# Performance work log

Hardware: AMD Instinct MI355X
Metric: run time of the kernel (lower is better)

Reference implementation:

```python
import jax, jax.numpy as jnp
import numpy as np

N_NODES = 100000
N_EDGES = 1600000
IN_DIM = 128
OUT_DIM = 64


def setup_inputs() -> dict:
    key = jax.random.key(0)
    k = jax.random.split(key, 6)
    h = jax.random.normal(k[0], (N_NODES, IN_DIM), dtype=jnp.float32)
    W_fc = jax.random.normal(k[1], (IN_DIM, OUT_DIM), dtype=jnp.float32) / np.float32(np.sqrt(IN_DIM))
    W_attn = jax.random.normal(k[2], (2 * OUT_DIM, 1), dtype=jnp.float32) / np.float32(np.sqrt(2 * OUT_DIM))
    W_edge = jax.random.normal(k[3], (2 * OUT_DIM, OUT_DIM), dtype=jnp.float32) / np.float32(np.sqrt(2 * OUT_DIM))
    src = jax.random.randint(k[4], (N_EDGES,), 0, N_NODES, dtype=jnp.int32)
    dst = jax.random.randint(k[5], (N_EDGES,), 0, N_NODES, dtype=jnp.int32)
    return {"h": h, "W_fc": W_fc, "W_attn": W_attn, "W_edge": W_edge, "src": src, "dst": dst}


def reference(h, W_fc, W_attn, W_edge, src, dst):
    # node projection: z = fc(h)
    z = h @ W_fc                                   # [N, out_dim]
    # gather per-edge src/dst features and concat (edge_type == 0 branch)
    z2 = jnp.concatenate([z[src], z[dst]], axis=1)  # [E, 2*out_dim]
    a = (z2 @ W_attn)[:, 0]                         # [E] attention logits
    e = z2 @ W_edge                                 # [E, out_dim] edge messages
    # segment softmax over incoming edges of each destination node
    a_max = jax.ops.segment_max(a, dst, num_segments=N_NODES)   # [N]
    w = jnp.exp(a - a_max[dst])                                  # [E]
    denom = jax.ops.segment_sum(w, dst, num_segments=N_NODES)    # [N]
    alpha = w / denom[dst]                                       # [E]
    # weighted scatter-add of neighbor features + sum of edge messages
    h1 = jax.ops.segment_sum(alpha[:, None] * z[src], dst, num_segments=N_NODES)
    h2 = jax.ops.segment_sum(e, dst, num_segments=N_NODES)
    return h1 + h2
```

## Files before the change

kernel.cpp:

```cpp
#include <hip/hip_runtime.h>

#define IN_DIM 128
#define OUT_DIM 64

#define NB 256
#define BSHIFT 9
#define NPB 512
#define EPT 16

typedef __attribute__((ext_vector_type(8))) short short8;
typedef __attribute__((ext_vector_type(4))) float f32x4;

__device__ __forceinline__ unsigned pack_bf16x2(float a, float b) {
    unsigned ua = __float_as_uint(a), ub = __float_as_uint(b);
    ua = (ua + 0x7fffu + ((ua >> 16) & 1u)) >> 16;
    ub = (ub + 0x7fffu + ((ub >> 16) & 1u)) >> 16;
    return ua | (ub << 16);
}

__global__ void precompute_weights(const float* __restrict__ W_fc,
                                   const float* __restrict__ W_edge,
                                   float* __restrict__ W1, float* __restrict__ W2) {
    int k = blockIdx.x;
    int j = threadIdx.x;
    __shared__ float row[64];
    row[j] = W_fc[k * 64 + j];
    __syncthreads();
    float s1 = 0.f, s2 = 0.f;
    #pragma unroll 8
    for (int m = 0; m < 64; ++m) {
        float w = row[m];
        s1 = fmaf(w, W_edge[m * 64 + j], s1);
        s2 = fmaf(w, W_edge[(64 + m) * 64 + j], s2);
    }
    W1[k * 64 + j] = s1;
    W2[k * 64 + j] = s2;
}

__global__ void pack_bfrags(const float* __restrict__ W_fc, const float* __restrict__ W1,
                            const float* __restrict__ W2, unsigned* __restrict__ bfrag) {
    int slot = blockIdx.x * 256 + threadIdx.x;
    if (slot >= 12 * 4 * 64) return;
    int lane = slot & 63;
    int ks = (slot >> 6) & 3;
    int t = slot >> 8;
    int grp = t >> 2;
    int col = (t & 3) * 16 + (lane & 15);
    int kbase = ks * 32 + (lane >> 4) * 8;
    const float* W = (grp == 0) ? W_fc : ((grp == 1) ? W1 : W2);
    unsigned o0 = pack_bf16x2(W[(kbase + 0) * 64 + col], W[(kbase + 1) * 64 + col]);
    unsigned o1 = pack_bf16x2(W[(kbase + 2) * 64 + col], W[(kbase + 3) * 64 + col]);
    unsigned o2 = pack_bf16x2(W[(kbase + 4) * 64 + col], W[(kbase + 5) * 64 + col]);
    unsigned o3 = pack_bf16x2(W[(kbase + 6) * 64 + col], W[(kbase + 7) * 64 + col]);
    ((uint4*)bfrag)[slot] = make_uint4(o0, o1, o2, o3);
}

__global__ __launch_bounds__(256) void node_gemm(
    const float* __restrict__ h, const unsigned* __restrict__ bfrag,
    const float* __restrict__ W_attn,
    unsigned* __restrict__ zes, float* __restrict__ ed,
    float* __restrict__ ws_, int N)
{
    __shared__ uint4 lds4[1024];
    char* lds = (char*)lds4;
    const int tid = threadIdx.x;
    const int lane = tid & 63;
    const int w = tid >> 6;
    const int n0 = blockIdx.x * 64;

    #pragma unroll
    for (int r = 0; r < 8; ++r) {
        int idx = r * 256 + tid;
        int row = idx >> 5;
        int c4 = idx & 31;
        float4 v = make_float4(0.f, 0.f, 0.f, 0.f);
        int n = n0 + row;
        if (n < N) v = *(const float4*)(h + (size_t)n * IN_DIM + c4 * 4);
        int byte = (row << 8) + (c4 << 3);
        byte ^= ((row & 7) << 4);
        *(uint2*)(lds + byte) = make_uint2(pack_bf16x2(v.x, v.y), pack_bf16x2(v.z, v.w));
    }
    __syncthreads();

    const int g = lane >> 4;
    const int c = lane & 15;

    union U { uint4 u; short8 s; };
    U a[4];
    {
        const int arow = (w << 4) + c;
        #pragma unroll
        for (int ks = 0; ks < 4; ++ks) {
            int byte = (arow << 8) + (ks << 6) + (g << 4);
            byte ^= ((arow & 7) << 4);
            a[ks].u = *(const uint4*)(lds + byte);
        }
    }

    f32x4 acc[12];
    #pragma unroll
    for (int t = 0; t < 12; ++t) acc[t] = (f32x4){0.f, 0.f, 0.f, 0.f};

    const uint4* bf4 = (const uint4*)bfrag;
    #pragma unroll
    for (int t = 0; t < 12; ++t) {
        #pragma unroll
        for (int ks = 0; ks < 4; ++ks) {
            U b; b.u = bf4[(t * 4 + ks) * 64 + lane];
            acc[t] = __builtin_amdgcn_mfma_f32_16x16x32_bf16(a[ks].s, b.s, acc[t], 0, 0, 0);
        }
    }

    const float wa0 = W_attn[c], wa1 = W_attn[16 + c], wa2 = W_attn[32 + c], wa3 = W_attn[48 + c];
    #pragma unroll
    for (int r = 0; r < 4; ++r) {
        const int n = n0 + (w << 4) + (g << 2) + r;
        float part = acc[0][r] * wa0 + acc[1][r] * wa1 + acc[2][r] * wa2 + acc[3][r] * wa3;
        part += __shfl_xor(part, 1);
        part += __shfl_xor(part, 2);
        part += __shfl_xor(part, 4);
        part += __shfl_xor(part, 8);
        if (n <= N) {
            #pragma unroll
            for (int t = 0; t < 4; ++t) {
                const int col = t * 16 + c;
                zes[(size_t)n * 64 + col] = pack_bf16x2(acc[t][r], acc[t + 4][r]);
                ed [(size_t)n * 64 + col] = acc[t + 8][r];
            }
            if (c == 0) ws_[n] = expf(part);
        }
    }
}

__global__ __launch_bounds__(256) void coarse_hist(const int* __restrict__ dst,
                                                   unsigned* __restrict__ hist, int E) {
    __shared__ unsigned hl[NB];
    const int t = threadIdx.x;
    hl[t] = 0;
    __syncthreads();
    const int base = blockIdx.x * (256 * EPT);
    const int lim = min(base + 256 * EPT, E);
    for (int i = base + t; i < lim; i += 256)
        atomicAdd(&hl[((unsigned)dst[i]) >> BSHIFT], 1u);
    __syncthreads();
    if (hl[t]) atomicAdd(&hist[t], hl[t]);
}

__global__ void bucket_scan(const unsigned* __restrict__ hist,
                            unsigned* __restrict__ bucketBase, unsigned* __restrict__ cursor) {
    __shared__ unsigned s[NB];
    const int t = threadIdx.x;
    unsigned v = hist[t];
    s[t] = v; __syncthreads();
    for (int off = 1; off < NB; off <<= 1) {
        unsigned add = (t >= off) ? s[t - off] : 0u;
        __syncthreads();
        s[t] += add;
        __syncthreads();
    }
    unsigned excl = s[t] - v;
    bucketBase[t] = excl;
    cursor[t] = excl;
    if (t == NB - 1) bucketBase[NB] = s[t];
}

__global__ __launch_bounds__(256) void coarse_scatter(
    const int* __restrict__ src, const int* __restrict__ dst,
    unsigned* __restrict__ cursor, unsigned* __restrict__ pairs, int E)
{
    __shared__ unsigned h[NB];
    __shared__ unsigned start[NB];
    const int t = threadIdx.x;
    h[t] = 0;
    __syncthreads();
    const int base = blockIdx.x * (256 * EPT);
    unsigned pv[EPT], bk[EPT], rk[EPT];
    #pragma unroll
    for (int k = 0; k < EPT; ++k) {
        int i = base + k * 256 + t;
        bool valid = i < E;
        unsigned s = 0, d = 0;
        if (valid) { s = (unsigned)src[i]; d = (unsigned)dst[i]; }
        pv[k] = (s << BSHIFT) | (d & (NPB - 1));
        bk[k] = valid ? (d >> BSHIFT) : 0xFFFFFFFFu;
        rk[k] = valid ? atomicAdd(&h[d >> BSHIFT], 1u) : 0u;
    }
    __syncthreads();
    start[t] = h[t] ? atomicAdd(&cursor[t], h[t]) : 0u;
    __syncthreads();
    #pragma unroll
    for (int k = 0; k < EPT; ++k) {
        if (bk[k] != 0xFFFFFFFFu)
            pairs[start[bk[k]] + rk[k]] = pv[k];
    }
}

__global__ __launch_bounds__(256) void fine_bin(
    const unsigned* __restrict__ pairs, const unsigned* __restrict__ bucketBase,
    unsigned* __restrict__ offs, int* __restrict__ srcoff_sorted, int N, int E)
{
    __shared__ unsigned deg[NPB];
    __shared__ unsigned excl[NPB];
    __shared__ unsigned pscan[256];
    const int b = blockIdx.x;
    const int t = threadIdx.x;
    const int node0 = b << BSHIFT;
    const unsigned e0 = bucketBase[b], e1 = bucketBase[b + 1];

    deg[t] = 0; deg[t + 256] = 0;
    __syncthreads();
    for (unsigned i = e0 + t; i < e1; i += 256)
        atomicAdd(&deg[pairs[i] & (NPB - 1)], 1u);
    __syncthreads();

    unsigned a0 = deg[2 * t], a1 = deg[2 * t + 1];
    unsigned ps = a0 + a1;
    pscan[t] = ps;
    __syncthreads();
    for (int off = 1; off < 256; off <<= 1) {
        unsigned add = (t >= off) ? pscan[t - off] : 0u;
        __syncthreads();
        pscan[t] += add;
        __syncthreads();
    }
    unsigned exclP = pscan[t] - ps;
    excl[2 * t] = exclP;
    excl[2 * t + 1] = exclP + a0;
    __syncthreads();

    #pragma unroll
    for (int l = t; l < NPB; l += 256) {
        int n = node0 + l;
        if (n < N) offs[n] = e0 + excl[l];
    }
    if (b == 0 && t == 0) offs[N] = (unsigned)E;
    __syncthreads();

    for (unsigned i = e0 + t; i < e1; i += 256) {
        unsigned p = pairs[i];
        unsigned loc = p & (NPB - 1);
        unsigned pos = e0 + atomicAdd(&excl[loc], 1u);
        srcoff_sorted[pos] = (int)((p >> BSHIFT) << 8);
    }
}

__global__ __launch_bounds__(256) void gather_nodes(
    const int* __restrict__ srcoff_sorted, const unsigned* __restrict__ offs,
    const float* __restrict__ ws_, const unsigned* __restrict__ zes,
    const float* __restrict__ ed, float* __restrict__ out, int N)
{
    const int lane = threadIdx.x & 63;
    const int l16 = lane & 15;
    const int gbase4 = (lane & 48) << 2;
    const int c4off = l16 << 4;
    const int d = blockIdx.x * 16 + (threadIdx.x >> 4);
    if (d >= N) return;
    const unsigned o0 = offs[d], o1 = offs[d + 1];
    const int deg = (int)(o1 - o0);
    const int zoff = N << 8;
    const char* zesb = (const char*)zes;

    float az0 = 0.f, az1 = 0.f, az2 = 0.f, az3 = 0.f;
    float ae0 = 0.f, ae1 = 0.f, ae2 = 0.f, ae3 = 0.f;
    float lsum = 0.f;

    for (unsigned base = o0; base < o1; base += 16) {
        const int rem = min(16, (int)(o1 - base));
        int soff = zoff; float w = 0.f;
        if (l16 < rem) { soff = srcoff_sorted[base + l16]; w = ws_[(unsigned)soff >> 8]; }
        lsum += w;
        const int e_end = (rem + 3) & ~3;
        for (int e = 0; e < e_end; e += 4) {
            int so[4]; float wg[4];
            #pragma unroll
            for (int k = 0; k < 4; ++k) {
                const int idx4 = gbase4 + ((e + k) << 2);
                so[k] = __builtin_amdgcn_ds_bpermute(idx4, soff);
                wg[k] = __uint_as_float(
                    (unsigned)__builtin_amdgcn_ds_bpermute(idx4, (int)__float_as_uint(w)));
            }
            uint4 u[4];
            #pragma unroll
            for (int k = 0; k < 4; ++k)
                u[k] = *(const uint4*)(zesb + (unsigned)(so[k] + c4off));
            #pragma unroll
            for (int k = 0; k < 4; ++k) {
                az0 = fmaf(wg[k], __uint_as_float(u[k].x << 16), az0); ae0 += __uint_as_float(u[k].x & 0xffff0000u);
                az1 = fmaf(wg[k], __uint_as_float(u[k].y << 16), az1); ae1 += __uint_as_float(u[k].y & 0xffff0000u);
                az2 = fmaf(wg[k], __uint_as_float(u[k].z << 16), az2); ae2 += __uint_as_float(u[k].z & 0xffff0000u);
                az3 = fmaf(wg[k], __uint_as_float(u[k].w << 16), az3); ae3 += __uint_as_float(u[k].w & 0xffff0000u);
            }
        }
    }

    lsum += __shfl_xor(lsum, 1);
    lsum += __shfl_xor(lsum, 2);
    lsum += __shfl_xor(lsum, 4);
    lsum += __shfl_xor(lsum, 8);

    const float inv = (lsum > 0.f) ? 1.f / lsum : 0.f;
    const float4 edv = *(const float4*)&ed[(size_t)d * 64 + l16 * 4];
    float4 r;
    r.x = fmaf((float)deg, edv.x, fmaf(az0, inv, ae0));
    r.y = fmaf((float)deg, edv.y, fmaf(az1, inv, ae1));
    r.z = fmaf((float)deg, edv.z, fmaf(az2, inv, ae2));
    r.w = fmaf((float)deg, edv.w, fmaf(az3, inv, ae3));
    *(float4*)&out[(size_t)d * 64 + l16 * 4] = r;
}

extern "C" void kernel_launch(void* const* d_in, const int* in_sizes, int n_in,
                              void* d_out, int out_size, void* d_ws, size_t ws_size,
                              hipStream_t stream) {
    const float* h      = (const float*)d_in[0];
    const float* W_fc   = (const float*)d_in[1];
    const float* W_attn = (const float*)d_in[2];
    const float* W_edge = (const float*)d_in[3];
    const int*   src    = (const int*)d_in[4];
    const int*   dst    = (const int*)d_in[5];
    float* out = (float*)d_out;

    const int N = in_sizes[0] / IN_DIM;
    const int E = in_sizes[4];

    char* p = (char*)d_ws;
    auto alloc = [&](size_t bytes) -> void* {
        void* r = (void*)p;
        p += (bytes + 255) & ~(size_t)255;
        return r;
    };
    unsigned* zes    = (unsigned*)alloc((size_t)(N + 1) * 64 * 4);
    float*    ed     = (float*)alloc((size_t)(N + 1) * 64 * 4);
    float*    ws_    = (float*)alloc((size_t)(N + 1) * 4);
    unsigned* offs   = (unsigned*)alloc((size_t)(N + 1) * 4);
    unsigned* hist   = (unsigned*)alloc(NB * 4);
    unsigned* bbase  = (unsigned*)alloc((NB + 1) * 4);
    unsigned* cursor = (unsigned*)alloc(NB * 4);
    unsigned* pairs  = (unsigned*)alloc((size_t)E * 4);
    int*      src_s  = (int*)alloc((size_t)E * 4);
    float*    W1     = (float*)alloc(128 * 64 * 4);
    float*    W2     = (float*)alloc(128 * 64 * 4);
    unsigned* bfrag  = (unsigned*)alloc((size_t)12 * 4 * 64 * 16);

    hipMemsetAsync(hist, 0, NB * 4, stream);

    precompute_weights<<<128, 64, 0, stream>>>(W_fc, W_edge, W1, W2);
    pack_bfrags<<<12, 256, 0, stream>>>(W_fc, W1, W2, bfrag);

    int blocksA = (N + 63) / 64;
    node_gemm<<<blocksA, 256, 0, stream>>>(h, bfrag, W_attn, zes, ed, ws_, N);

    int blocksC = (E + 256 * EPT - 1) / (256 * EPT);
    coarse_hist<<<blocksC, 256, 0, stream>>>(dst, hist, E);
    bucket_scan<<<1, NB, 0, stream>>>(hist, bbase, cursor);
    coarse_scatter<<<blocksC, 256, 0, stream>>>(src, dst, cursor, pairs, E);
    fine_bin<<<NB, 256, 0, stream>>>(pairs, bbase, offs, src_s, N, E);

    gather_nodes<<<(N + 15) / 16, 256, 0, stream>>>(src_s, offs, ws_, zes, ed, out, N);
}
```

Before: 252.5 us.

## Fuse weight precompute, histogram and scan into fewer launches; store ed as bf16

Folds the W_fc·W_edge product into pack_bfrags and merges coarse_hist and bucket_scan into the node GEMM kernel as extra blocks, with a last-block-done counter triggering the scan. This cuts the number of kernel launches. It also halves EPT, runs fine_bin with 1024 threads per block, and stores the per-node edge term as bf16 to halve its write and read traffic. The costs are lower precision on the edge term and reliance on threadfence and atomic ordering for the fused scan.

```diff
diff --git a/kernel.cpp b/kernel.cpp
--- a/kernel.cpp
+++ b/kernel.cpp
@@ -6,7 +6,7 @@
 #define NB 256
 #define BSHIFT 9
 #define NPB 512
-#define EPT 16
+#define EPT 8
 
 typedef __attribute__((ext_vector_type(8))) short short8;
 typedef __attribute__((ext_vector_type(4))) float f32x4;
@@ -17,28 +17,14 @@
     ub = (ub + 0x7fffu + ((ub >> 16) & 1u)) >> 16;
     return ua | (ub << 16);
 }
-
-__global__ void precompute_weights(const float* __restrict__ W_fc,
-                                   const float* __restrict__ W_edge,
-                                   float* __restrict__ W1, float* __restrict__ W2) {
-    int k = blockIdx.x;
-    int j = threadIdx.x;
-    __shared__ float row[64];
-    row[j] = W_fc[k * 64 + j];
-    __syncthreads();
-    float s1 = 0.f, s2 = 0.f;
-    #pragma unroll 8
-    for (int m = 0; m < 64; ++m) {
-        float w = row[m];
-        s1 = fmaf(w, W_edge[m * 64 + j], s1);
-        s2 = fmaf(w, W_edge[(64 + m) * 64 + j], s2);
-    }
-    W1[k * 64 + j] = s1;
-    W2[k * 64 + j] = s2;
-}
-
-__global__ void pack_bfrags(const float* __restrict__ W_fc, const float* __restrict__ W1,
-                            const float* __restrict__ W2, unsigned* __restrict__ bfrag) {
+__device__ __forceinline__ unsigned short bf16_1(float a) {
+    unsigned ua = __float_as_uint(a);
+    ua = (ua + 0x7fffu + ((ua >> 16) & 1u)) >> 16;
+    return (unsigned short)ua;
+}
+
+__global__ void pack_bfrags(const float* __restrict__ W_fc, const float* __restrict__ W_edge,
+                            unsigned* __restrict__ bfrag) {
     int slot = blockIdx.x * 256 + threadIdx.x;
     if (slot >= 12 * 4 * 64) return;
     int lane = slot & 63;
@@ -47,26 +33,76 @@
     int grp = t >> 2;
     int col = (t & 3) * 16 + (lane & 15);
     int kbase = ks * 32 + (lane >> 4) * 8;
-    const float* W = (grp == 0) ? W_fc : ((grp == 1) ? W1 : W2);
-    unsigned o0 = pack_bf16x2(W[(kbase + 0) * 64 + col], W[(kbase + 1) * 64 + col]);
-    unsigned o1 = pack_bf16x2(W[(kbase + 2) * 64 + col], W[(kbase + 3) * 64 + col]);
-    unsigned o2 = pack_bf16x2(W[(kbase + 4) * 64 + col], W[(kbase + 5) * 64 + col]);
-    unsigned o3 = pack_bf16x2(W[(kbase + 6) * 64 + col], W[(kbase + 7) * 64 + col]);
+    float vals[8];
+    if (grp == 0) {
+        #pragma unroll
+        for (int j = 0; j < 8; ++j) vals[j] = W_fc[(kbase + j) * 64 + col];
+    } else {
+        const float* We = W_edge + (grp == 1 ? 0 : 64 * 64);
+        #pragma unroll
+        for (int j = 0; j < 8; ++j) {
+            float s = 0.f;
+            for (int m = 0; m < 64; ++m)
+                s = fmaf(W_fc[(kbase + j) * 64 + m], We[m * 64 + col], s);
+            vals[j] = s;
+        }
+    }
+    unsigned o0 = pack_bf16x2(vals[0], vals[1]);
+    unsigned o1 = pack_bf16x2(vals[2], vals[3]);
+    unsigned o2 = pack_bf16x2(vals[4], vals[5]);
+    unsigned o3 = pack_bf16x2(vals[6], vals[7]);
     ((uint4*)bfrag)[slot] = make_uint4(o0, o1, o2, o3);
 }
 
-__global__ __launch_bounds__(256) void node_gemm(
+__global__ __launch_bounds__(256) void combo(
     const float* __restrict__ h, const unsigned* __restrict__ bfrag,
     const float* __restrict__ W_attn,
-    unsigned* __restrict__ zes, float* __restrict__ ed,
-    float* __restrict__ ws_, int N)
+    unsigned* __restrict__ zes, unsigned short* __restrict__ ed16,
+    float* __restrict__ ws_, int N,
+    const int* __restrict__ dst, unsigned* __restrict__ hist,
+    unsigned* __restrict__ bucketBase, unsigned* __restrict__ cursor,
+    int E, int blocksH)
 {
-    __shared__ uint4 lds4[1024];
-    char* lds = (char*)lds4;
+    __shared__ uint4 shmem[1024];
     const int tid = threadIdx.x;
+
+    if ((int)blockIdx.x < blocksH) {
+        unsigned* hl = (unsigned*)shmem;
+        unsigned* sscan = (unsigned*)shmem + NB;
+        unsigned* flag = (unsigned*)shmem + 2 * NB;
+        unsigned* done = hist + NB;
+        hl[tid] = 0;
+        __syncthreads();
+        const int base = blockIdx.x * (256 * EPT);
+        const int lim = min(base + 256 * EPT, E);
+        for (int i = base + tid; i < lim; i += 256)
+            atomicAdd(&hl[((unsigned)dst[i]) >> BSHIFT], 1u);
+        __syncthreads();
+        if (hl[tid]) atomicAdd(&hist[tid], hl[tid]);
+        __threadfence();
+        if (tid == 0) *flag = (atomicAdd(done, 1u) == (unsigned)(blocksH - 1)) ? 1u : 0u;
+        __syncthreads();
+        if (!*flag) return;
+        unsigned v = atomicAdd(&hist[tid], 0u);
+        sscan[tid] = v;
+        __syncthreads();
+        for (int off = 1; off < NB; off <<= 1) {
+            unsigned add = (tid >= off) ? sscan[tid - off] : 0u;
+            __syncthreads();
+            sscan[tid] += add;
+            __syncthreads();
+        }
+        unsigned excl = sscan[tid] - v;
+        bucketBase[tid] = excl;
+        cursor[tid] = excl;
+        if (tid == NB - 1) bucketBase[NB] = sscan[tid];
+        return;
+    }
+
+    char* lds = (char*)shmem;
     const int lane = tid & 63;
     const int w = tid >> 6;
-    const int n0 = blockIdx.x * 64;
+    const int n0 = ((int)blockIdx.x - blocksH) * 64;
 
     #pragma unroll
     for (int r = 0; r < 8; ++r) {
@@ -124,44 +160,12 @@
             #pragma unroll
             for (int t = 0; t < 4; ++t) {
                 const int col = t * 16 + c;
-                zes[(size_t)n * 64 + col] = pack_bf16x2(acc[t][r], acc[t + 4][r]);
-                ed [(size_t)n * 64 + col] = acc[t + 8][r];
+                zes [(size_t)n * 64 + col] = pack_bf16x2(acc[t][r], acc[t + 4][r]);
+                ed16[(size_t)n * 64 + col] = bf16_1(acc[t + 8][r]);
             }
             if (c == 0) ws_[n] = expf(part);
         }
     }
-}
-
-__global__ __launch_bounds__(256) void coarse_hist(const int* __restrict__ dst,
-                                                   unsigned* __restrict__ hist, int E) {
-    __shared__ unsigned hl[NB];
-    const int t = threadIdx.x;
-    hl[t] = 0;
-    __syncthreads();
-    const int base = blockIdx.x * (256 * EPT);
-    const int lim = min(base + 256 * EPT, E);
-    for (int i = base + t; i < lim; i += 256)
-        atomicAdd(&hl[((unsigned)dst[i]) >> BSHIFT], 1u);
-    __syncthreads();
-    if (hl[t]) atomicAdd(&hist[t], hl[t]);
-}
-
-__global__ void bucket_scan(const unsigned* __restrict__ hist,
-                            unsigned* __restrict__ bucketBase, unsigned* __restrict__ cursor) {
-    __shared__ unsigned s[NB];
-    const int t = threadIdx.x;
-    unsigned v = hist[t];
-    s[t] = v; __syncthreads();
-    for (int off = 1; off < NB; off <<= 1) {
-        unsigned add = (t >= off) ? s[t - off] : 0u;
-        __syncthreads();
-        s[t] += add;
-        __syncthreads();
-    }
-    unsigned excl = s[t] - v;
-    bucketBase[t] = excl;
-    cursor[t] = excl;
-    if (t == NB - 1) bucketBase[NB] = s[t];
 }
 
 __global__ __launch_bounds__(256) void coarse_scatter(
@@ -195,7 +199,7 @@
     }
 }
 
-__global__ __launch_bounds__(256) void fine_bin(
+__global__ __launch_bounds__(1024) void fine_bin(
     const unsigned* __restrict__ pairs, const unsigned* __restrict__ bucketBase,
     unsigned* __restrict__ offs, int* __restrict__ srcoff_sorted, int N, int E)
 {
@@ -207,39 +211,35 @@
     const int node0 = b << BSHIFT;
     const unsigned e0 = bucketBase[b], e1 = bucketBase[b + 1];
 
-    deg[t] = 0; deg[t + 256] = 0;
-    __syncthreads();
-    for (unsigned i = e0 + t; i < e1; i += 256)
+    if (t < NPB) deg[t] = 0;
+    __syncthreads();
+    for (unsigned i = e0 + t; i < e1; i += 1024)
         atomicAdd(&deg[pairs[i] & (NPB - 1)], 1u);
     __syncthreads();
 
-    unsigned a0 = deg[2 * t], a1 = deg[2 * t + 1];
-    unsigned ps = a0 + a1;
-    pscan[t] = ps;
+    unsigned a0 = 0, a1 = 0, ps = 0;
+    if (t < 256) { a0 = deg[2 * t]; a1 = deg[2 * t + 1]; ps = a0 + a1; pscan[t] = ps; }
     __syncthreads();
     for (int off = 1; off < 256; off <<= 1) {
-        unsigned add = (t >= off) ? pscan[t - off] : 0u;
-        __syncthreads();
-        pscan[t] += add;
-        __syncthreads();
-    }
-    unsigned exclP = pscan[t] - ps;
-    excl[2 * t] = exclP;
-    excl[2 * t + 1] = exclP + a0;
-    __syncthreads();
-
-    #pragma unroll
-    for (int l = t; l < NPB; l += 256) {
-        int n = node0 + l;
-        if (n < N) offs[n] = e0 + excl[l];
+        unsigned add = 0;
+        if (t < 256 && t >= off) add = pscan[t - off];
+        __syncthreads();
+        if (t < 256) pscan[t] += add;
+        __syncthreads();
+    }
+    if (t < 256) { unsigned ex = pscan[t] - ps; excl[2 * t] = ex; excl[2 * t + 1] = ex + a0; }
+    __syncthreads();
+
+    if (t < NPB) {
+        int n = node0 + t;
+        if (n < N) offs[n] = e0 + excl[t];
     }
     if (b == 0 && t == 0) offs[N] = (unsigned)E;
     __syncthreads();
 
-    for (unsigned i = e0 + t; i < e1; i += 256) {
+    for (unsigned i = e0 + t; i < e1; i += 1024) {
         unsigned p = pairs[i];
-        unsigned loc = p & (NPB - 1);
-        unsigned pos = e0 + atomicAdd(&excl[loc], 1u);
+        unsigned pos = e0 + atomicAdd(&excl[p & (NPB - 1)], 1u);
         srcoff_sorted[pos] = (int)((p >> BSHIFT) << 8);
     }
 }
@@ -247,7 +247,7 @@
 __global__ __launch_bounds__(256) void gather_nodes(
     const int* __restrict__ srcoff_sorted, const unsigned* __restrict__ offs,
     const float* __restrict__ ws_, const unsigned* __restrict__ zes,
-    const float* __restrict__ ed, float* __restrict__ out, int N)
+    const unsigned short* __restrict__ ed16, float* __restrict__ out, int N)
 {
     const int lane = threadIdx.x & 63;
     const int l16 = lane & 15;
@@ -299,12 +299,13 @@
     lsum += __shfl_xor(lsum, 8);
 
     const float inv = (lsum > 0.f) ? 1.f / lsum : 0.f;
-    const float4 edv = *(const float4*)&ed[(size_t)d * 64 + l16 * 4];
+    const ushort4 ev = *(const ushort4*)&ed16[(size_t)d * 64 + l16 * 4];
+    const float degf = (float)deg;
     float4 r;
-    r.x = fmaf((float)deg, edv.x, fmaf(az0, inv, ae0));
-    r.y = fmaf((float)deg, edv.y, fmaf(az1, inv, ae1));
-    r.z = fmaf((float)deg, edv.z, fmaf(az2, inv, ae2));
-    r.w = fmaf((float)deg, edv.w, fmaf(az3, inv, ae3));
+    r.x = fmaf(degf, __uint_as_float((unsigned)ev.x << 16), fmaf(az0, inv, ae0));
+    r.y = fmaf(degf, __uint_as_float((unsigned)ev.y << 16), fmaf(az1, inv, ae1));
+    r.z = fmaf(degf, __uint_as_float((unsigned)ev.z << 16), fmaf(az2, inv, ae2));
+    r.w = fmaf(degf, __uint_as_float((unsigned)ev.w << 16), fmaf(az3, inv, ae3));
     *(float4*)&out[(size_t)d * 64 + l16 * 4] = r;
 }
 
@@ -328,32 +329,28 @@
         p += (bytes + 255) & ~(size_t)255;
         return r;
     };
-    unsigned* zes    = (unsigned*)alloc((size_t)(N + 1) * 64 * 4);
-    float*    ed     = (float*)alloc((size_t)(N + 1) * 64 * 4);
-    float*    ws_    = (float*)alloc((size_t)(N + 1) * 4);
-    unsigned* offs   = (unsigned*)alloc((size_t)(N + 1) * 4);
-    unsigned* hist   = (unsigned*)alloc(NB * 4);
-    unsigned* bbase  = (unsigned*)alloc((NB + 1) * 4);
-    unsigned* cursor = (unsigned*)alloc(NB * 4);
-    unsigned* pairs  = (unsigned*)alloc((size_t)E * 4);
-    int*      src_s  = (int*)alloc((size_t)E * 4);
-    float*    W1     = (float*)alloc(128 * 64 * 4);
-    float*    W2     = (float*)alloc(128 * 64 * 4);
-    unsigned* bfrag  = (unsigned*)alloc((size_t)12 * 4 * 64 * 16);
-
-    hipMemsetAsync(hist, 0, NB * 4, stream);
-
-    precompute_weights<<<128, 64, 0, stream>>>(W_fc, W_edge, W1, W2);
-    pack_bfrags<<<12, 256, 0, stream>>>(W_fc, W1, W2, bfrag);
-
-    int blocksA = (N + 63) / 64;
-    node_gemm<<<blocksA, 256, 0, stream>>>(h, bfrag, W_attn, zes, ed, ws_, N);
-
-    int blocksC = (E + 256 * EPT - 1) / (256 * EPT);
-    coarse_hist<<<blocksC, 256, 0, stream>>>(dst, hist, E);
-    bucket_scan<<<1, NB, 0, stream>>>(hist, bbase, cursor);
-    coarse_scatter<<<blocksC, 256, 0, stream>>>(src, dst, cursor, pairs, E);
-    fine_bin<<<NB, 256, 0, stream>>>(pairs, bbase, offs, src_s, N, E);
-
-    gather_nodes<<<(N + 15) / 16, 256, 0, stream>>>(src_s, offs, ws_, zes, ed, out, N);
-}
+    unsigned*       zes    = (unsigned*)alloc((size_t)(N + 1) * 64 * 4);
+    unsigned short* ed16   = (unsigned short*)alloc((size_t)(N + 1) * 64 * 2);
+    float*          ws_    = (float*)alloc((size_t)(N + 1) * 4);
+    unsigned*       offs   = (unsigned*)alloc((size_t)(N + 1) * 4);
+    unsigned*       hist   = (unsigned*)alloc((NB + 1) * 4);
+    unsigned*       bbase  = (unsigned*)alloc((NB + 1) * 4);
+    unsigned*       cursor = (unsigned*)alloc(NB * 4);
+    unsigned*       pairs  = (unsigned*)alloc((size_t)E * 4);
+    int*            src_s  = (int*)alloc((size_t)E * 4);
+    unsigned*       bfrag  = (unsigned*)alloc((size_t)12 * 4 * 64 * 16);
+
+    hipMemsetAsync(hist, 0, (NB + 1) * 4, stream);
+
+    pack_bfrags<<<12, 256, 0, stream>>>(W_fc, W_edge, bfrag);
+
+    const int blocksA = (N + 63) / 64;
+    const int blocksH = (E + 256 * EPT - 1) / (256 * EPT);
+    combo<<<blocksH + blocksA, 256, 0, stream>>>(h, bfrag, W_attn, zes, ed16, ws_, N,
+                                                 dst, hist, bbase, cursor, E, blocksH);
+
+    coarse_scatter<<<blocksH, 256, 0, stream>>>(src, dst, cursor, pairs, E);
+    fine_bin<<<NB, 1024, 0, stream>>>(pairs, bbase, offs, src_s, N, E);
+
+    gather_nodes<<<(N + 15) / 16, 256, 0, stream>>>(src_s, offs, ws_, zes, ed16, out, N);
+}
```

New measurement: 297.4 us. 1.18x slower.
